# Optimization experiments

Measured on AMD Instinct MI355X. Metric: run time of the kernel, lower is better.

## Reference

```python
import jax, jax.numpy as jnp
import numpy as np

LATENT = 2000
N_GROUPS = 10000  # loci_count // window_size
KERNEL = 20       # window_size * 2; per-group input length is 1 so out length == KERNEL
BATCH = 128
EPS = 1e-5
SLOPE = 0.1


def setup_inputs() -> dict:
    key = jax.random.key(0)
    k1, k2, k3, k4, k5 = jax.random.split(key, 5)
    return {
        "z": jax.random.normal(k1, (BATCH, LATENT), dtype=jnp.float32),
        "W_fc": jax.random.normal(k2, (N_GROUPS, LATENT), dtype=jnp.float32) * 0.02,
        "b_fc": jax.random.normal(k3, (N_GROUPS,), dtype=jnp.float32) * 0.02,
        "gamma": jnp.ones((N_GROUPS,), dtype=jnp.float32),
        "beta": jnp.zeros((N_GROUPS,), dtype=jnp.float32),
        "conv_w": jax.random.normal(k4, (N_GROUPS, KERNEL), dtype=jnp.float32) * 0.1,
        "conv_b": jax.random.normal(k5, (N_GROUPS,), dtype=jnp.float32) * 0.02,
    }


def reference(z, W_fc, b_fc, gamma, beta, conv_w, conv_b):
    # Linear: (B, L) @ (L, G) -> (B, G)
    h = jnp.einsum("bl,gl->bg", z, W_fc) + b_fc
    # BatchNorm1d (training mode: biased batch statistics, eps=1e-5)
    mean = jnp.mean(h, axis=0)
    var = jnp.mean(jnp.square(h - mean), axis=0)
    h = (h - mean) * jax.lax.rsqrt(var + EPS) * gamma + beta
    h = jnp.where(h >= 0, h, SLOPE * h)  # LeakyReLU(0.1)
    # Grouped ConvTranspose1d with per-group input length 1 degenerates to
    # an outer product per channel: y[b,g,k] = h[b,g]*w[g,k] + b[g]
    y = h[:, :, None] * conv_w[None, :, :] + conv_b[None, :, None]  # (B, G, K)
    y = jnp.where(y >= 0, y, SLOPE * y)  # LeakyReLU(0.1)
    out = jax.nn.sigmoid(y.reshape(z.shape[0], N_GROUPS * KERNEL))
    return out
```

## Files before the change

kernel.cpp:

```cpp
#include <hip/hip_runtime.h>
#include <hip/hip_bf16.h>
#include <stdint.h>

#define BATCH 128
#define LAT   2000
#define NG    10000
#define KW    20
#define OUTW  (NG * KW)
#define EPSV  1e-5f

#define GT    64
#define BK    64
#define KSPL  4

typedef __bf16 bf16x8 __attribute__((ext_vector_type(8)));
typedef float  f32x4  __attribute__((ext_vector_type(4)));

__device__ __forceinline__ ushort f2bf(float f) {
  uint32_t u = __builtin_bit_cast(uint32_t, f);
  u = (u + 0x7FFFu + ((u >> 16) & 1u)) >> 16;
  return (ushort)u;
}

__device__ __forceinline__ int4 pack8(const float* p) {
  float4 f0 = *(const float4*)p;
  float4 f1 = *(const float4*)(p + 4);
  int4 v;
  v.x = (int)((uint32_t)f2bf(f0.x) | ((uint32_t)f2bf(f0.y) << 16));
  v.y = (int)((uint32_t)f2bf(f0.z) | ((uint32_t)f2bf(f0.w) << 16));
  v.z = (int)((uint32_t)f2bf(f1.x) | ((uint32_t)f2bf(f1.y) << 16));
  v.w = (int)((uint32_t)f2bf(f1.z) | ((uint32_t)f2bf(f1.w) << 16));
  return v;
}

__global__ __launch_bounds__(256, 4) void gemm_splitk_kernel(
    const float* __restrict__ zp, const float* __restrict__ wp,
    float* __restrict__ hp) {
  const int tid = threadIdx.x;
  const int g0  = blockIdx.x * GT;
  const int s   = blockIdx.y;
  const int kbase = s * 512;
  const int klen  = (s < 3) ? 512 : (LAT - 3 * 512);

  __shared__ ushort As[GT * BK];
  __shared__ ushort Bs[BATCH * BK];

  const int lane = tid & 63;
  const int w    = tid >> 6;
  const int wm   = w & 1;
  const int wn   = w >> 1;
  const int q    = lane >> 4;
  const int cl   = lane & 15;

  f32x4 acc[2][4];
  const f32x4 vzero = {0.f, 0.f, 0.f, 0.f};
#pragma unroll
  for (int i = 0; i < 2; ++i)
#pragma unroll
    for (int j = 0; j < 4; ++j) acc[i][j] = vzero;

  for (int it = 0; it < 8; ++it) {
    const int k0 = it * BK;
    __syncthreads();

#pragma unroll
    for (int i = 0; i < 2; ++i) {
      int c = i * 256 + tid;
      int r = c >> 3, sc = c & 7;
      int lk = k0 + sc * 8;
      int g  = g0 + r;
      int4 v = make_int4(0, 0, 0, 0);
      if (lk < klen && g < NG)
        v = pack8(wp + (size_t)g * LAT + kbase + lk);
      *(int4*)&As[r * BK + ((sc ^ (r & 7)) << 3)] = v;
    }
#pragma unroll
    for (int i = 0; i < 4; ++i) {
      int c = i * 256 + tid;
      int r = c >> 3, sc = c & 7;
      int lk = k0 + sc * 8;
      int4 v = make_int4(0, 0, 0, 0);
      if (lk < klen)
        v = pack8(zp + (size_t)r * LAT + kbase + lk);
      *(int4*)&Bs[r * BK + ((sc ^ (r & 7)) << 3)] = v;
    }
    __syncthreads();

#pragma unroll
    for (int kk = 0; kk < 2; ++kk) {
      int sc = kk * 4 + q;
      bf16x8 af[2], bfr[4];
#pragma unroll
      for (int mt = 0; mt < 2; ++mt) {
        int ra = wm * 32 + mt * 16 + cl;
        af[mt] = *(const bf16x8*)&As[ra * BK + ((sc ^ (ra & 7)) << 3)];
      }
#pragma unroll
      for (int nt = 0; nt < 4; ++nt) {
        int rb = wn * 64 + nt * 16 + cl;
        bfr[nt] = *(const bf16x8*)&Bs[rb * BK + ((sc ^ (rb & 7)) << 3)];
      }
#pragma unroll
      for (int mt = 0; mt < 2; ++mt)
#pragma unroll
        for (int nt = 0; nt < 4; ++nt)
          acc[mt][nt] = __builtin_amdgcn_mfma_f32_16x16x32_bf16(
              af[mt], bfr[nt], acc[mt][nt], 0, 0, 0);
    }
  }

  float* base = hp + (size_t)s * NG * BATCH;
#pragma unroll
  for (int mt = 0; mt < 2; ++mt) {
#pragma unroll
    for (int r = 0; r < 4; ++r) {
      int g = g0 + wm * 32 + mt * 16 + q * 4 + r;
      if (g < NG) {
#pragma unroll
        for (int nt = 0; nt < 4; ++nt) {
          int b = wn * 64 + nt * 16 + cl;
          base[(size_t)g * BATCH + b] = acc[mt][nt][r];
        }
      }
    }
  }
}

__global__ __launch_bounds__(256, 4) void stats_kernel(
    const float* __restrict__ hp, const float* __restrict__ gammap,
    const float* __restrict__ betap, float* __restrict__ scalep,
    float* __restrict__ shiftp) {
  const int tid = threadIdx.x;
  const int g   = blockIdx.x * 8 + (tid >> 5);
  const int l32 = tid & 31;

  float4 hv = make_float4(0.f, 0.f, 0.f, 0.f);
#pragma unroll
  for (int s = 0; s < KSPL; ++s) {
    float4 v = *(const float4*)(hp + ((size_t)s * NG + g) * BATCH + l32 * 4);
    hv.x += v.x; hv.y += v.y; hv.z += v.z; hv.w += v.w;
  }
  float sm = hv.x + hv.y + hv.z + hv.w;
  float sq = hv.x * hv.x + hv.y * hv.y + hv.z * hv.z + hv.w * hv.w;
#pragma unroll
  for (int m = 1; m < 32; m <<= 1) {
    sm += __shfl_xor(sm, m);
    sq += __shfl_xor(sq, m);
  }
  if (l32 == 0) {
    float mean = sm * (1.f / 128.f);
    float var  = sq * (1.f / 128.f) - mean * mean;
    var = (var < 0.f) ? 0.f : var;
    float inv   = __builtin_amdgcn_rsqf(var + EPSV);
    float scale = inv * gammap[g];
    scalep[g] = scale;
    shiftp[g] = betap[g] - mean * scale;
  }
}

__global__ __launch_bounds__(256, 4) void expand_kernel(
    const float* __restrict__ hp, const float* __restrict__ scalep,
    const float* __restrict__ shiftp, const float* __restrict__ convwp,
    const float* __restrict__ convbp, float* __restrict__ out) {
  const int tid = threadIdx.x;
  const int g   = blockIdx.x * 8 + (tid >> 5);
  const int bc  = (tid & 31) * 4;

  float4 hv = make_float4(0.f, 0.f, 0.f, 0.f);
#pragma unroll
  for (int s = 0; s < KSPL; ++s) {
    float4 v = *(const float4*)(hp + ((size_t)s * NG + g) * BATCH + bc);
    hv.x += v.x; hv.y += v.y; hv.z += v.z; hv.w += v.w;
  }

  const float scale = scalep[g];
  const float shift = shiftp[g];
  const float cb    = convbp[g];
  float wv[KW];
  {
    const float4* pw = (const float4*)(convwp + (size_t)g * KW);
#pragma unroll
    for (int j = 0; j < 5; ++j) {
      float4 f = pw[j];
      wv[4 * j] = f.x; wv[4 * j + 1] = f.y;
      wv[4 * j + 2] = f.z; wv[4 * j + 3] = f.w;
    }
  }

  float hb[4] = {hv.x, hv.y, hv.z, hv.w};
#pragma unroll
  for (int i = 0; i < 4; ++i) {
    float h = hb[i] * scale + shift;
    h = fmaxf(h, h * 0.1f);
    float4 ov[5];
#pragma unroll
    for (int j = 0; j < 5; ++j) {
      float y0 = h * wv[4 * j]     + cb;
      float y1 = h * wv[4 * j + 1] + cb;
      float y2 = h * wv[4 * j + 2] + cb;
      float y3 = h * wv[4 * j + 3] + cb;
      y0 = fmaxf(y0, y0 * 0.1f);
      y1 = fmaxf(y1, y1 * 0.1f);
      y2 = fmaxf(y2, y2 * 0.1f);
      y3 = fmaxf(y3, y3 * 0.1f);
      ov[j].x = __builtin_amdgcn_rcpf(1.f + exp2f(y0 * -1.44269504f));
      ov[j].y = __builtin_amdgcn_rcpf(1.f + exp2f(y1 * -1.44269504f));
      ov[j].z = __builtin_amdgcn_rcpf(1.f + exp2f(y2 * -1.44269504f));
      ov[j].w = __builtin_amdgcn_rcpf(1.f + exp2f(y3 * -1.44269504f));
    }
    float4* po = (float4*)(out + (size_t)(bc + i) * OUTW + (size_t)g * KW);
#pragma unroll
    for (int j = 0; j < 5; ++j) po[j] = ov[j];
  }
}

__global__ __launch_bounds__(256, 2) void fused_decoder_kernel(
    const float* __restrict__ zp, const float* __restrict__ wp,
    const float* __restrict__ gammap, const float* __restrict__ betap,
    const float* __restrict__ convwp, const float* __restrict__ convbp,
    float* __restrict__ out) {
  const int tid = threadIdx.x;
  const int g0  = blockIdx.x * 32;

  __shared__ ushort As[BATCH * BK];
  __shared__ ushort Bs[32 * BK];
  __shared__ float statS[2][2][16];
  __shared__ float statQ[2][2][16];

  const int lane = tid & 63;
  const int w    = tid >> 6;
  const int wm   = w & 1;
  const int wn   = w >> 1;
  const int q    = lane >> 4;
  const int cl   = lane & 15;

  f32x4 acc[4];
  const f32x4 vzero = {0.f, 0.f, 0.f, 0.f};
#pragma unroll
  for (int i = 0; i < 4; ++i) acc[i] = vzero;

  for (int it = 0; it < 32; ++it) {
    const int k0 = it * BK;
    __syncthreads();
#pragma unroll
    for (int i = 0; i < 4; ++i) {
      int c = i * 256 + tid;
      int r = c >> 3, sc = c & 7;
      int gk = k0 + sc * 8;
      int4 v = make_int4(0, 0, 0, 0);
      if (gk < LAT) v = pack8(zp + (size_t)r * LAT + gk);
      *(int4*)&As[r * BK + ((sc ^ (r & 7)) << 3)] = v;
    }
    {
      int r = tid >> 3, sc = tid & 7;
      int g  = g0 + r;
      int gk = k0 + sc * 8;
      int4 v = make_int4(0, 0, 0, 0);
      if (gk < LAT && g < NG) v = pack8(wp + (size_t)g * LAT + gk);
      *(int4*)&Bs[r * BK + ((sc ^ (r & 7)) << 3)] = v;
    }
    __syncthreads();
#pragma unroll
    for (int kk = 0; kk < 2; ++kk) {
      int sc = kk * 4 + q;
      bf16x8 af[4], bfr;
#pragma unroll
      for (int mt = 0; mt < 4; ++mt) {
        int ra = wm * 64 + mt * 16 + cl;
        af[mt] = *(const bf16x8*)&As[ra * BK + ((sc ^ (ra & 7)) << 3)];
      }
      {
        int rb = wn * 16 + cl;
        bfr = *(const bf16x8*)&Bs[rb * BK + ((sc ^ (rb & 7)) << 3)];
      }
#pragma unroll
      for (int mt = 0; mt < 4; ++mt)
        acc[mt] = __builtin_amdgcn_mfma_f32_16x16x32_bf16(af[mt], bfr,
                                                          acc[mt], 0, 0, 0);
    }
  }

  float s = 0.f, ss = 0.f;
#pragma unroll
  for (int mt = 0; mt < 4; ++mt)
#pragma unroll
    for (int r = 0; r < 4; ++r) {
      float v = acc[mt][r];
      s += v; ss += v * v;
    }
  s += __shfl_xor(s, 16); ss += __shfl_xor(ss, 16);
  s += __shfl_xor(s, 32); ss += __shfl_xor(ss, 32);
  if (q == 0) { statS[wm][wn][cl] = s; statQ[wm][wn][cl] = ss; }
  __syncthreads();

  const int gcol = g0 + wn * 16 + cl;
  const int gc   = (gcol < NG) ? gcol : (NG - 1);
  float S = statS[0][wn][cl] + statS[1][wn][cl];
  float Q = statQ[0][wn][cl] + statQ[1][wn][cl];
  float mean = S * (1.f / 128.f);
  float var  = Q * (1.f / 128.f) - mean * mean;
  var = (var < 0.f) ? 0.f : var;
  float inv = __builtin_amdgcn_rsqf(var + EPSV);
  float ga = gammap[gc], be = betap[gc], cb = convbp[gc];
  float wv[KW];
  {
    const float4* pw = (const float4*)(convwp + (size_t)gc * KW);
#pragma unroll
    for (int j = 0; j < 5; ++j) {
      float4 f = pw[j];
      wv[4 * j] = f.x; wv[4 * j + 1] = f.y;
      wv[4 * j + 2] = f.z; wv[4 * j + 3] = f.w;
    }
  }
  float scale = inv * ga;
  float shift = be - mean * scale;
  const bool ok = (gcol < NG);
#pragma unroll
  for (int mt = 0; mt < 4; ++mt) {
#pragma unroll
    for (int r = 0; r < 4; ++r) {
      float h = acc[mt][r] * scale + shift;
      h = fmaxf(h, h * 0.1f);
      int b = wm * 64 + mt * 16 + q * 4 + r;
      float4 ov[5];
#pragma unroll
      for (int j = 0; j < 5; ++j) {
        float y0 = h * wv[4 * j]     + cb;
        float y1 = h * wv[4 * j + 1] + cb;
        float y2 = h * wv[4 * j + 2] + cb;
        float y3 = h * wv[4 * j + 3] + cb;
        y0 = fmaxf(y0, y0 * 0.1f);
        y1 = fmaxf(y1, y1 * 0.1f);
        y2 = fmaxf(y2, y2 * 0.1f);
        y3 = fmaxf(y3, y3 * 0.1f);
        ov[j].x = __builtin_amdgcn_rcpf(1.f + exp2f(y0 * -1.44269504f));
        ov[j].y = __builtin_amdgcn_rcpf(1.f + exp2f(y1 * -1.44269504f));
        ov[j].z = __builtin_amdgcn_rcpf(1.f + exp2f(y2 * -1.44269504f));
        ov[j].w = __builtin_amdgcn_rcpf(1.f + exp2f(y3 * -1.44269504f));
      }
      if (ok) {
        float4* po = (float4*)(out + (size_t)b * OUTW + (size_t)gcol * KW);
#pragma unroll
        for (int j = 0; j < 5; ++j) po[j] = ov[j];
      }
    }
  }
}

extern "C" void kernel_launch(void* const* d_in, const int* in_sizes, int n_in,
                              void* d_out, int out_size, void* d_ws, size_t ws_size,
                              hipStream_t stream) {
  const float* z     = (const float*)d_in[0];
  const float* W     = (const float*)d_in[1];
  const float* gamma = (const float*)d_in[3];
  const float* beta  = (const float*)d_in[4];
  const float* convw = (const float*)d_in[5];
  const float* convb = (const float*)d_in[6];
  float* out = (float*)d_out;

  const size_t hp_elems = (size_t)KSPL * NG * BATCH;
  const size_t need = (hp_elems + 2 * NG) * sizeof(float);

  if (ws_size >= need) {
    float* hp     = (float*)d_ws;
    float* scalep = hp + hp_elems;
    float* shiftp = scalep + NG;

    dim3 g1((NG + GT - 1) / GT, KSPL);
    gemm_splitk_kernel<<<g1, 256, 0, stream>>>(z, W, hp);
    stats_kernel<<<NG / 8, 256, 0, stream>>>(hp, gamma, beta, scalep, shiftp);
    expand_kernel<<<NG / 8, 256, 0, stream>>>(hp, scalep, shiftp, convw,
                                              convb, out);
  } else {
    fused_decoder_kernel<<<(NG + 31) / 32, 256, 0, stream>>>(
        z, W, gamma, beta, convw, convb, out);
  }
}
```

Baseline: 225.1 us.

## Pre-convert z to bf16, deepen split-K, fold BN stats into expand kernel

Adds a small kernel that converts z to bf16 once, so GEMM blocks load packed bf16 instead of converting fp32 on every tile. Raises split-K from 4 to 8 segments of 256, doubling the number of GEMM blocks for better occupancy, at the cost of twice the partial-sum traffic. Drops the separate stats kernel and computes BatchNorm mean and variance inside the expand kernel via wave shuffles, removing a launch and the scale/shift round trip. The expand kernel now sums 8 partials per element instead of 4.

```diff
diff --git a/kernel.cpp b/kernel.cpp
--- a/kernel.cpp
+++ b/kernel.cpp
@@ -11,7 +11,8 @@
 
 #define GT    64
 #define BK    64
-#define KSPL  4
+#define KSPL  8
+#define KSEG  256
 
 typedef __bf16 bf16x8 __attribute__((ext_vector_type(8)));
 typedef float  f32x4  __attribute__((ext_vector_type(4)));
@@ -33,14 +34,21 @@
   return v;
 }
 
+__global__ __launch_bounds__(256, 4) void convert_z_kernel(
+    const float* __restrict__ zp, ushort* __restrict__ zb) {
+  const int idx = (blockIdx.x * 256 + threadIdx.x) * 8;
+  int4 v = pack8(zp + idx);
+  *(int4*)(zb + idx) = v;
+}
+
 __global__ __launch_bounds__(256, 4) void gemm_splitk_kernel(
-    const float* __restrict__ zp, const float* __restrict__ wp,
+    const ushort* __restrict__ zb, const float* __restrict__ wp,
     float* __restrict__ hp) {
   const int tid = threadIdx.x;
   const int g0  = blockIdx.x * GT;
   const int s   = blockIdx.y;
-  const int kbase = s * 512;
-  const int klen  = (s < 3) ? 512 : (LAT - 3 * 512);
+  const int kbase = s * KSEG;
+  const int klen  = (s < KSPL - 1) ? KSEG : (LAT - (KSPL - 1) * KSEG);
 
   __shared__ ushort As[GT * BK];
   __shared__ ushort Bs[BATCH * BK];
@@ -59,7 +67,7 @@
 #pragma unroll
     for (int j = 0; j < 4; ++j) acc[i][j] = vzero;
 
-  for (int it = 0; it < 8; ++it) {
+  for (int it = 0; it < KSEG / BK; ++it) {
     const int k0 = it * BK;
     __syncthreads();
 
@@ -81,7 +89,7 @@
       int lk = k0 + sc * 8;
       int4 v = make_int4(0, 0, 0, 0);
       if (lk < klen)
-        v = pack8(zp + (size_t)r * LAT + kbase + lk);
+        v = *(const int4*)(zb + (size_t)r * LAT + kbase + lk);
       *(int4*)&Bs[r * BK + ((sc ^ (r & 7)) << 3)] = v;
     }
     __syncthreads();
@@ -126,41 +134,9 @@
   }
 }
 
-__global__ __launch_bounds__(256, 4) void stats_kernel(
+__global__ __launch_bounds__(256, 4) void expand_kernel(
     const float* __restrict__ hp, const float* __restrict__ gammap,
-    const float* __restrict__ betap, float* __restrict__ scalep,
-    float* __restrict__ shiftp) {
-  const int tid = threadIdx.x;
-  const int g   = blockIdx.x * 8 + (tid >> 5);
-  const int l32 = tid & 31;
-
-  float4 hv = make_float4(0.f, 0.f, 0.f, 0.f);
-#pragma unroll
-  for (int s = 0; s < KSPL; ++s) {
-    float4 v = *(const float4*)(hp + ((size_t)s * NG + g) * BATCH + l32 * 4);
-    hv.x += v.x; hv.y += v.y; hv.z += v.z; hv.w += v.w;
-  }
-  float sm = hv.x + hv.y + hv.z + hv.w;
-  float sq = hv.x * hv.x + hv.y * hv.y + hv.z * hv.z + hv.w * hv.w;
-#pragma unroll
-  for (int m = 1; m < 32; m <<= 1) {
-    sm += __shfl_xor(sm, m);
-    sq += __shfl_xor(sq, m);
-  }
-  if (l32 == 0) {
-    float mean = sm * (1.f / 128.f);
-    float var  = sq * (1.f / 128.f) - mean * mean;
-    var = (var < 0.f) ? 0.f : var;
-    float inv   = __builtin_amdgcn_rsqf(var + EPSV);
-    float scale = inv * gammap[g];
-    scalep[g] = scale;
-    shiftp[g] = betap[g] - mean * scale;
-  }
-}
-
-__global__ __launch_bounds__(256, 4) void expand_kernel(
-    const float* __restrict__ hp, const float* __restrict__ scalep,
-    const float* __restrict__ shiftp, const float* __restrict__ convwp,
+    const float* __restrict__ betap, const float* __restrict__ convwp,
     const float* __restrict__ convbp, float* __restrict__ out) {
   const int tid = threadIdx.x;
   const int g   = blockIdx.x * 8 + (tid >> 5);
@@ -173,9 +149,21 @@
     hv.x += v.x; hv.y += v.y; hv.z += v.z; hv.w += v.w;
   }
 
-  const float scale = scalep[g];
-  const float shift = shiftp[g];
-  const float cb    = convbp[g];
+  float sm = hv.x + hv.y + hv.z + hv.w;
+  float sq = hv.x * hv.x + hv.y * hv.y + hv.z * hv.z + hv.w * hv.w;
+#pragma unroll
+  for (int m = 1; m < 32; m <<= 1) {
+    sm += __shfl_xor(sm, m);
+    sq += __shfl_xor(sq, m);
+  }
+  float mean = sm * (1.f / 128.f);
+  float var  = sq * (1.f / 128.f) - mean * mean;
+  var = (var < 0.f) ? 0.f : var;
+  float inv   = __builtin_amdgcn_rsqf(var + EPSV);
+  float scale = inv * gammap[g];
+  float shift = betap[g] - mean * scale;
+  const float cb = convbp[g];
+
   float wv[KW];
   {
     const float4* pw = (const float4*)(convwp + (size_t)g * KW);
@@ -359,17 +347,16 @@
   float* out = (float*)d_out;
 
   const size_t hp_elems = (size_t)KSPL * NG * BATCH;
-  const size_t need = (hp_elems + 2 * NG) * sizeof(float);
+  const size_t need = hp_elems * 4 + (size_t)BATCH * LAT * 2;
 
   if (ws_size >= need) {
-    float* hp     = (float*)d_ws;
-    float* scalep = hp + hp_elems;
-    float* shiftp = scalep + NG;
-
+    float*  hp = (float*)d_ws;
+    ushort* zb = (ushort*)(hp + hp_elems);
+
+    convert_z_kernel<<<BATCH * LAT / (256 * 8), 256, 0, stream>>>(z, zb);
     dim3 g1((NG + GT - 1) / GT, KSPL);
-    gemm_splitk_kernel<<<g1, 256, 0, stream>>>(z, W, hp);
-    stats_kernel<<<NG / 8, 256, 0, stream>>>(hp, gamma, beta, scalep, shiftp);
-    expand_kernel<<<NG / 8, 256, 0, stream>>>(hp, scalep, shiftp, convw,
+    gemm_splitk_kernel<<<g1, 256, 0, stream>>>(zb, W, hp);
+    expand_kernel<<<NG / 8, 256, 0, stream>>>(hp, gamma, beta, convw,
                                               convb, out);
   } else {
     fused_decoder_kernel<<<(NG + 31) / 32, 256, 0, stream>>>(
```

New measurement: 232.5 us. +3.3%, slower.
